# Kernel optimization log

Hardware: AMD Instinct MI355X
Metric: run time of the kernel (lower is better)

## Reference

```python
import jax, jax.numpy as jnp
import numpy as np

EMB_DIM = 2048
N_Q_HEADS = 32
N_KV_HEADS = 8
HEAD_DIM = EMB_DIM // N_Q_HEADS  # 64
N_REP = N_Q_HEADS // N_KV_HEADS  # 4
ROPE_BASE = 10000.0


def setup_inputs() -> dict:
    key = jax.random.key(0)
    ks = jax.random.split(key, 9)
    B, T = 2, 2048
    kv_dim = HEAD_DIM * N_KV_HEADS
    s = 0.02
    return {
        "x":  jax.random.normal(ks[0], (B, T, EMB_DIM), jnp.float32),
        "Wq": jax.random.normal(ks[1], (EMB_DIM, EMB_DIM), jnp.float32) * s,
        "bq": jax.random.normal(ks[2], (EMB_DIM,), jnp.float32) * s,
        "Wk": jax.random.normal(ks[3], (kv_dim, EMB_DIM), jnp.float32) * s,
        "bk": jax.random.normal(ks[4], (kv_dim,), jnp.float32) * s,
        "Wv": jax.random.normal(ks[5], (kv_dim, EMB_DIM), jnp.float32) * s,
        "bv": jax.random.normal(ks[6], (kv_dim,), jnp.float32) * s,
        "Wo": jax.random.normal(ks[7], (EMB_DIM, EMB_DIM), jnp.float32) * s,
        "bo": jax.random.normal(ks[8], (EMB_DIM,), jnp.float32) * s,
    }


def _rope_tables(T, D, dtype):
    inv_freq = 1.0 / (ROPE_BASE ** (jnp.arange(0, D, 2, dtype=jnp.float32) / D))
    t = jnp.arange(T, dtype=jnp.float32)
    freqs = jnp.einsum("i,j->ij", t, inv_freq)          # [T, D/2]
    emb = jnp.concatenate([freqs, freqs], axis=-1)       # [T, D]
    # broadcast over batch and heads: [1, T, 1, D]
    return jnp.cos(emb)[None, :, None, :].astype(dtype), jnp.sin(emb)[None, :, None, :].astype(dtype)


def _rotate_half(x):
    x1, x2 = jnp.split(x, 2, axis=-1)
    return jnp.concatenate([-x2, x1], axis=-1)


def reference(x, Wq, bq, Wk, bk, Wv, bv, Wo, bo):
    B, T, C = x.shape
    q = (x @ Wq.T + bq).reshape(B, T, N_Q_HEADS, HEAD_DIM)
    k = (x @ Wk.T + bk).reshape(B, T, N_KV_HEADS, HEAD_DIM)
    v = (x @ Wv.T + bv).reshape(B, T, N_KV_HEADS, HEAD_DIM)

    cos, sin = _rope_tables(T, HEAD_DIM, x.dtype)
    q = q * cos + _rotate_half(q) * sin
    k = k * cos + _rotate_half(k) * sin

    q = q.transpose(0, 2, 1, 3)                          # [B, Hq, T, D]
    k = k.transpose(0, 2, 1, 3)                          # [B, Hkv, T, D]
    v = v.transpose(0, 2, 1, 3)
    # GQA: repeat_interleave kv heads to match query heads
    k = jnp.repeat(k, N_REP, axis=1)                     # [B, Hq, T, D]
    v = jnp.repeat(v, N_REP, axis=1)

    scale = 1.0 / jnp.sqrt(jnp.asarray(HEAD_DIM, x.dtype))
    att = jnp.einsum("bhqd,bhkd->bhqk", q, k) * scale    # [B, Hq, T, T]
    causal = jnp.tril(jnp.ones((T, T), dtype=bool))
    att = jnp.where(causal[None, None], att, -jnp.inf)
    att = jax.nn.softmax(att, axis=-1)

    y = jnp.einsum("bhqk,bhkd->bhqd", att, v)            # [B, Hq, T, D]
    y = y.transpose(0, 2, 1, 3).reshape(B, T, C)
    return y @ Wo.T + bo
```

## Files before the change

### kernel.cpp

```cpp
#include <hip/hip_runtime.h>
#include <hip/hip_bf16.h>
#include <math.h>


typedef __attribute__((ext_vector_type(8))) short short8;
typedef __attribute__((ext_vector_type(4))) float f32x4;

#define MFMA16(a,b,c) __builtin_amdgcn_mfma_f32_16x16x32_bf16((a),(b),(c),0,0,0)
#define QSCALE 0.18033688011112043f
#define NFREQ  (-13.28771237954945f / 32.0f)

__device__ __forceinline__ ushort f2bf(float f) {
  union { float f; unsigned u; } x; x.f = f;
  unsigned r = x.u + 0x7fffu + ((x.u >> 16) & 1u);
  return (ushort)(r >> 16);
}
__device__ __forceinline__ uint pkbf(float a, float b) {
  union { float f; unsigned u; } x, y; x.f = a; y.f = b;
  return ((x.u + 0x8000u) >> 16) | ((y.u + 0x8000u) & 0xffff0000u);
}

__device__ __forceinline__ void g2l16(const void* g, void* l) {
  __builtin_amdgcn_global_load_lds(
      (__attribute__((address_space(1))) void*)g,
      (__attribute__((address_space(3))) void*)l, 16, 0, 0);
}

__global__ void cvt_all(const float* __restrict__ x,  const float* __restrict__ wq,
                        const float* __restrict__ wk, const float* __restrict__ wv,
                        const float* __restrict__ wo,
                        ushort* __restrict__ x_bf, ushort* __restrict__ wqkv,
                        ushort* __restrict__ wo_bf) {
  int i = blockIdx.x * 256 + threadIdx.x;
  const float4* src; ushort* dst; int off;
  if (i < 2097152)      { src = (const float4*)x;  dst = x_bf;             off = i; }
  else if (i < 3145728) { src = (const float4*)wq; dst = wqkv;             off = i - 2097152; }
  else if (i < 3407872) { src = (const float4*)wk; dst = wqkv + 4194304;   off = i - 3145728; }
  else if (i < 3670016) { src = (const float4*)wv; dst = wqkv + 5242880;   off = i - 3407872; }
  else                  { src = (const float4*)wo; dst = wo_bf;            off = i - 3670016; }
  float4 v = src[off];
  ushort4 o;
  o.x = f2bf(v.x); o.y = f2bf(v.y); o.z = f2bf(v.z); o.w = f2bf(v.w);
  ((ushort4*)dst)[off] = o;
}

__global__ __launch_bounds__(256, 3)
void gemm_qkv(const ushort* __restrict__ A, const ushort* __restrict__ Bw,
              const float* __restrict__ bq, const float* __restrict__ bk,
              const float* __restrict__ bv,
              ushort* __restrict__ qr, ushort* __restrict__ kr,
              ushort* __restrict__ vt) {
  const int K = 2048;
  __shared__ ushort As[2][128*32];
  __shared__ ushort Bs[2][128*32];
  const int tid = threadIdx.x;
  const int wave = tid >> 6, lane = tid & 63;
  const int wm = wave >> 1, wn = wave & 1;
  const int quad = lane >> 4, l16 = lane & 15;
  const int swg = (l16 >> 1) & 3;
  const int m0 = blockIdx.y * 128, n0 = blockIdx.x * 128;

  f32x4 acc[4][4] = {};

  auto stage = [&](int buf, int k0) {
#pragma unroll
    for (int i = 0; i < 2; ++i) {
      int cbase = (i*4 + wave) * 64;
      int p = cbase + lane;
      int row = p >> 2, pcb = p & 3;
      int cl = pcb ^ ((row >> 1) & 3);
      g2l16(A  + (size_t)(m0 + row) * K + k0 + cl * 8, As[buf] + (size_t)cbase * 8);
      g2l16(Bw + (size_t)(n0 + row) * K + k0 + cl * 8, Bs[buf] + (size_t)cbase * 8);
    }
  };

  stage(0, 0);
  for (int k0 = 0; k0 < K; k0 += 32) {
    __syncthreads();
    int cur = (k0 >> 5) & 1;
    if (k0 + 32 < K) stage(cur ^ 1, k0 + 32);

    short8 af[4], bfr[4];
#pragma unroll
    for (int mi = 0; mi < 4; ++mi)
      af[mi] = *(const short8*)(As[cur] + (wm*64 + mi*16 + l16)*32 + ((quad ^ swg) * 8));
#pragma unroll
    for (int ni = 0; ni < 4; ++ni)
      bfr[ni] = *(const short8*)(Bs[cur] + (wn*64 + ni*16 + l16)*32 + ((quad ^ swg) * 8));
#pragma unroll
    for (int mi = 0; mi < 4; ++mi)
#pragma unroll
      for (int ni = 0; ni < 4; ++ni)
        acc[mi][ni] = MFMA16(af[mi], bfr[ni], acc[mi][ni]);
  }

  const int bb = m0 >> 11;
  const int tb = (m0 & 2047) + wm*64;

  if (blockIdx.x < 20) {
    const bool isq = blockIdx.x < 16;
    const float scale = isq ? QSCALE : 1.0f;
#pragma unroll
    for (int ni = 0; ni < 2; ++ni) {
      int n = n0 + wn*64 + ni*16 + l16;
      int d = ni*16 + l16;
      float bias1, bias2;
      ushort* dst;
      if (isq) {
        bias1 = bq[n]; bias2 = bq[n + 32];
        dst = qr + ((size_t)(bb*32 + (n >> 6)) * 2048) * 64 + d;
      } else {
        bias1 = bk[n - 2048]; bias2 = bk[n - 2016];
        dst = kr + ((size_t)(bb*8 + ((n >> 6) - 32)) * 2048) * 64 + d;
      }
      float invf = exp2f((float)d * NFREQ);
#pragma unroll
      for (int mi = 0; mi < 4; ++mi) {
#pragma unroll
        for (int r = 0; r < 4; ++r) {
          int t = tb + mi*16 + quad*4 + r;
          float x1 = acc[mi][ni][r]   + bias1;
          float x2 = acc[mi][ni+2][r] + bias2;
          float f = (float)t * invf;
          float sn = __sinf(f), cs = __cosf(f);
          dst[(size_t)t*64]      = f2bf((x1*cs - x2*sn) * scale);
          dst[(size_t)t*64 + 32] = f2bf((x2*cs + x1*sn) * scale);
        }
      }
    }
  } else {
#pragma unroll
    for (int ni = 0; ni < 4; ++ni) {
      int n = n0 + wn*64 + ni*16 + l16;
      int d = ni*16 + l16;
      float bias = bv[n - 2560];
      ushort* dst = vt + ((size_t)(bb*8 + ((n - 2560) >> 6)) * 64 + d) * 2048;
#pragma unroll
      for (int mi = 0; mi < 4; ++mi) {
        int t = tb + mi*16 + quad*4;
        uint2 pk;
        pk.x = (uint)f2bf(acc[mi][ni][0]+bias) | ((uint)f2bf(acc[mi][ni][1]+bias) << 16);
        pk.y = (uint)f2bf(acc[mi][ni][2]+bias) | ((uint)f2bf(acc[mi][ni][3]+bias) << 16);
        *(uint2*)(dst + t) = pk;
      }
    }
  }
}

__global__ __launch_bounds__(256, 3)
void gemm128(const ushort* __restrict__ A, const ushort* __restrict__ Bw,
             const float* __restrict__ b0,
             float* __restrict__ Cout, int M, int N, int K) {
  __shared__ ushort As[2][128*32];
  __shared__ ushort Bs[2][128*32];
  const int tid = threadIdx.x;
  const int wave = tid >> 6, lane = tid & 63;
  const int wm = wave >> 1, wn = wave & 1;
  const int quad = lane >> 4, l16 = lane & 15;
  const int swg = (l16 >> 1) & 3;
  const int m0 = blockIdx.y * 128, n0 = blockIdx.x * 128;

  f32x4 acc[4][4] = {};

  auto stage = [&](int buf, int k0) {
#pragma unroll
    for (int i = 0; i < 2; ++i) {
      int cbase = (i*4 + wave) * 64;
      int p = cbase + lane;
      int row = p >> 2, pcb = p & 3;
      int cl = pcb ^ ((row >> 1) & 3);
      g2l16(A  + (size_t)(m0 + row) * K + k0 + cl * 8, As[buf] + (size_t)cbase * 8);
      g2l16(Bw + (size_t)(n0 + row) * K + k0 + cl * 8, Bs[buf] + (size_t)cbase * 8);
    }
  };

  stage(0, 0);
  for (int k0 = 0; k0 < K; k0 += 32) {
    __syncthreads();
    int cur = (k0 >> 5) & 1;
    if (k0 + 32 < K) stage(cur ^ 1, k0 + 32);

    short8 af[4], bfr[4];
#pragma unroll
    for (int mi = 0; mi < 4; ++mi)
      af[mi] = *(const short8*)(As[cur] + (wm*64 + mi*16 + l16)*32 + ((quad ^ swg) * 8));
#pragma unroll
    for (int ni = 0; ni < 4; ++ni)
      bfr[ni] = *(const short8*)(Bs[cur] + (wn*64 + ni*16 + l16)*32 + ((quad ^ swg) * 8));
#pragma unroll
    for (int mi = 0; mi < 4; ++mi)
#pragma unroll
      for (int ni = 0; ni < 4; ++ni)
        acc[mi][ni] = MFMA16(af[mi], bfr[ni], acc[mi][ni]);
  }

#pragma unroll
  for (int ni = 0; ni < 4; ++ni) {
    int n = n0 + wn*64 + ni*16 + l16;
    float bias = b0[n];
#pragma unroll
    for (int mi = 0; mi < 4; ++mi) {
#pragma unroll
      for (int r = 0; r < 4; ++r) {
        int m = m0 + wm*64 + mi*16 + quad*4 + r;
        Cout[(size_t)m * N + n] = acc[mi][ni][r] + bias;
      }
    }
  }
}

__global__ __launch_bounds__(256, 4)
void attn(const ushort* __restrict__ Q, const ushort* __restrict__ Kb,
          const ushort* __restrict__ Vt, ushort* __restrict__ Y) {
  __shared__ ushort Ks[2][64*64];
  __shared__ ushort Vs[2][64*64];
  __shared__ ushort Ps[4*16*64];
  const int tid = threadIdx.x, wave = tid >> 6, lane = tid & 63;
  const int quad = lane >> 4, l16 = lane & 15;
  const int h = blockIdx.y, b = blockIdx.z;
  const int hk = h >> 2;
  const ushort* Qb = Q  + ((size_t)(b*32 + h)  * 2048) * 64;
  const ushort* Kg = Kb + ((size_t)(b*8 + hk) * 2048) * 64;
  const ushort* Vg = Vt + ((size_t)(b*8 + hk) * 64) * 2048;
  ushort* Pw = Ps + wave * 1024;
  const int sw = l16 & 7;

  auto stage = [&](int buf, int kt) {
#pragma unroll
    for (int i = 0; i < 2; ++i) {
      int cbase = (i*4 + wave) * 64;
      int p = cbase + lane;
      int row = p >> 3, pcb = p & 7;
      int cl = pcb ^ (row & 7);
      g2l16(Kg + (size_t)(kt*64 + row)*64 + cl*8, Ks[buf] + (size_t)cbase*8);
      g2l16(Vg + (size_t)row*2048 + kt*64 + cl*8, Vs[buf] + (size_t)cbase*8);
    }
  };

  for (int pass = 0; pass < 2; ++pass) {
    const int qt = pass ? (31 - blockIdx.x) : blockIdx.x;
    const int q0 = qt * 64;
    const int qrow = q0 + wave*16 + l16;
    short8 qf0 = *(const short8*)(Qb + (size_t)qrow*64 + quad*8);
    short8 qf1 = *(const short8*)(Qb + (size_t)qrow*64 + 32 + quad*8);

    f32x4 o[4] = {};
    f32x4 l4 = {0.f, 0.f, 0.f, 0.f};

    __syncthreads();
    stage(0, 0);

    for (int kt = 0; kt <= qt; ++kt) {
      __syncthreads();
      int cur = kt & 1;
      if (kt < qt) stage(cur ^ 1, kt + 1);

      f32x4 s[4];
#pragma unroll
      for (int kb = 0; kb < 4; ++kb) {
        const ushort* krow = Ks[cur] + (kb*16 + l16)*64;
        short8 kf0 = *(const short8*)(krow + ((quad       ^ sw) * 8));
        short8 kf1 = *(const short8*)(krow + (((4 + quad) ^ sw) * 8));
        f32x4 z = {0.f, 0.f, 0.f, 0.f};
        z = MFMA16(kf0, qf0, z);
        s[kb] = MFMA16(kf1, qf1, z);
      }

      if (kt == qt) {
        int ql = wave*16 + l16;
#pragma unroll
        for (int kb = 0; kb < 4; ++kb) {
          int keyl = kb*16 + quad*4;
#pragma unroll
          for (int r = 0; r < 4; ++r)
            if (keyl + r > ql) s[kb][r] = -INFINITY;
        }
      }

#pragma unroll
      for (int kb = 0; kb < 4; ++kb)
#pragma unroll
        for (int r = 0; r < 4; ++r)
          s[kb][r] = __builtin_amdgcn_exp2f(s[kb][r]);

      l4 += (s[0] + s[1]) + (s[2] + s[3]);

#pragma unroll
      for (int kb = 0; kb < 4; ++kb) {
        uint2 pk;
        pk.x = pkbf(s[kb][0], s[kb][1]);
        pk.y = pkbf(s[kb][2], s[kb][3]);
        int G = (kb*2 + (quad >> 1)) ^ sw;
        *(uint2*)((char*)Pw + l16*128 + G*16 + (quad & 1)*8) = pk;
      }

#pragma unroll
      for (int kc = 0; kc < 2; ++kc) {
        short8 pf = *(const short8*)((char*)Pw + l16*128 + (((kc*4 + quad) ^ sw) * 16));
#pragma unroll
        for (int db = 0; db < 4; ++db) {
          const ushort* vrow = Vs[cur] + (db*16 + l16)*64;
          short8 vf = *(const short8*)(vrow + (((kc*4 + quad) ^ sw) * 8));
          o[db] = MFMA16(vf, pf, o[db]);
        }
      }
    }

    float l = (l4[0] + l4[1]) + (l4[2] + l4[3]);
    l += __shfl_xor(l, 16);
    l += __shfl_xor(l, 32);
    float inv = 1.0f / l;

    int q = q0 + wave*16 + l16;
#pragma unroll
    for (int db = 0; db < 4; ++db) {
      size_t base = ((size_t)(b*2048 + q)) * 2048 + h*64 + db*16 + quad*4;
      ((uint*)Y)[base >> 1]       = pkbf(o[db][0]*inv, o[db][1]*inv);
      ((uint*)Y)[(base >> 1) + 1] = pkbf(o[db][2]*inv, o[db][3]*inv);
    }
  }
}

extern "C" void kernel_launch(void* const* d_in, const int* in_sizes, int n_in,
                              void* d_out, int out_size, void* d_ws, size_t ws_size,
                              hipStream_t stream) {
  (void)in_sizes; (void)n_in; (void)out_size; (void)ws_size;
  const float* x  = (const float*)d_in[0];
  const float* Wq = (const float*)d_in[1];
  const float* bq = (const float*)d_in[2];
  const float* Wk = (const float*)d_in[3];
  const float* bk = (const float*)d_in[4];
  const float* Wv = (const float*)d_in[5];
  const float* bv = (const float*)d_in[6];
  const float* Wo = (const float*)d_in[7];
  const float* bo = (const float*)d_in[8];
  float* out = (float*)d_out;

  ushort* ws    = (ushort*)d_ws;
  ushort* x_bf  = ws;
  ushort* wqkv  = x_bf + 8388608;
  ushort* wo_bf = wqkv + 6291456;
  ushort* qr    = wo_bf + 4194304;
  ushort* kr    = qr + 8388608;
  ushort* vt    = kr + 2097152;
  ushort* Y     = x_bf;

  cvt_all<<<18432, 256, 0, stream>>>(x, Wq, Wk, Wv, Wo, x_bf, wqkv, wo_bf);
  gemm_qkv<<<dim3(24, 32), 256, 0, stream>>>(x_bf, wqkv, bq, bk, bv, qr, kr, vt);
  attn<<<dim3(16, 32, 2), 256, 0, stream>>>(qr, kr, vt, Y);
  gemm128<<<dim3(16, 32), 256, 0, stream>>>(Y, wo_bf, bo, out, 4096, 2048, 2048);
}
```

Measured before the change: 295.2 us.

## Enlarge attention query tile to 128 rows and remap GEMM block order

The attention kernel moves to 512-thread blocks, each covering 128 query rows with 8 waves. Every staged K/V tile is now shared by twice as many waves, which halves the K/V traffic per query and halves the block count. It also adds s_setprio around the MFMA sections. Both GEMMs gain a block-index swizzle that groups neighbouring tiles to improve L2 reuse. The risks are lower occupancy from the larger blocks and extra masked work on the diagonal, since causal masking now spans two 64-key tiles.

Result: faster. 286.3 us (-3.0%).

```diff
diff --git a/kernel.cpp b/kernel.cpp
--- a/kernel.cpp
+++ b/kernel.cpp
@@ -58,7 +58,10 @@
   const int wm = wave >> 1, wn = wave & 1;
   const int quad = lane >> 4, l16 = lane & 15;
   const int swg = (l16 >> 1) & 3;
-  const int m0 = blockIdx.y * 128, n0 = blockIdx.x * 128;
+  int id = blockIdx.y * 24 + blockIdx.x;
+  id = (id & 7) * 96 + (id >> 3);
+  const int bx = id % 24, by = id / 24;
+  const int m0 = by * 128, n0 = bx * 128;
 
   f32x4 acc[4][4] = {};
 
@@ -97,8 +100,8 @@
   const int bb = m0 >> 11;
   const int tb = (m0 & 2047) + wm*64;
 
-  if (blockIdx.x < 20) {
-    const bool isq = blockIdx.x < 16;
+  if (bx < 20) {
+    const bool isq = bx < 16;
     const float scale = isq ? QSCALE : 1.0f;
 #pragma unroll
     for (int ni = 0; ni < 2; ++ni) {
@@ -158,7 +161,9 @@
   const int wm = wave >> 1, wn = wave & 1;
   const int quad = lane >> 4, l16 = lane & 15;
   const int swg = (l16 >> 1) & 3;
-  const int m0 = blockIdx.y * 128, n0 = blockIdx.x * 128;
+  int id = blockIdx.y * 16 + blockIdx.x;
+  id = (id & 7) * 64 + (id >> 3);
+  const int m0 = (id / 16) * 128, n0 = (id % 16) * 128;
 
   f32x4 acc[4][4] = {};
 
@@ -209,12 +214,12 @@
   }
 }
 
-__global__ __launch_bounds__(256, 4)
+__global__ __launch_bounds__(512, 4)
 void attn(const ushort* __restrict__ Q, const ushort* __restrict__ Kb,
           const ushort* __restrict__ Vt, ushort* __restrict__ Y) {
   __shared__ ushort Ks[2][64*64];
   __shared__ ushort Vs[2][64*64];
-  __shared__ ushort Ps[4*16*64];
+  __shared__ ushort Ps[8*16*64];
   const int tid = threadIdx.x, wave = tid >> 6, lane = tid & 63;
   const int quad = lane >> 4, l16 = lane & 15;
   const int h = blockIdx.y, b = blockIdx.z;
@@ -226,20 +231,16 @@
   const int sw = l16 & 7;
 
   auto stage = [&](int buf, int kt) {
-#pragma unroll
-    for (int i = 0; i < 2; ++i) {
-      int cbase = (i*4 + wave) * 64;
-      int p = cbase + lane;
-      int row = p >> 3, pcb = p & 7;
-      int cl = pcb ^ (row & 7);
-      g2l16(Kg + (size_t)(kt*64 + row)*64 + cl*8, Ks[buf] + (size_t)cbase*8);
-      g2l16(Vg + (size_t)row*2048 + kt*64 + cl*8, Vs[buf] + (size_t)cbase*8);
-    }
+    int p = tid;
+    int row = p >> 3, pcb = p & 7;
+    int cl = pcb ^ (row & 7);
+    g2l16(Kg + (size_t)(kt*64 + row)*64 + cl*8, Ks[buf] + wave*512);
+    g2l16(Vg + (size_t)row*2048 + kt*64 + cl*8, Vs[buf] + wave*512);
   };
 
   for (int pass = 0; pass < 2; ++pass) {
-    const int qt = pass ? (31 - blockIdx.x) : blockIdx.x;
-    const int q0 = qt * 64;
+    const int qt = pass ? (15 - blockIdx.x) : blockIdx.x;
+    const int q0 = qt * 128;
     const int qrow = q0 + wave*16 + l16;
     short8 qf0 = *(const short8*)(Qb + (size_t)qrow*64 + quad*8);
     short8 qf1 = *(const short8*)(Qb + (size_t)qrow*64 + 32 + quad*8);
@@ -250,12 +251,14 @@
     __syncthreads();
     stage(0, 0);
 
-    for (int kt = 0; kt <= qt; ++kt) {
+    const int ktmax = qt*2 + 1;
+    for (int kt = 0; kt <= ktmax; ++kt) {
       __syncthreads();
       int cur = kt & 1;
-      if (kt < qt) stage(cur ^ 1, kt + 1);
+      if (kt < ktmax) stage(cur ^ 1, kt + 1);
 
       f32x4 s[4];
+      __builtin_amdgcn_s_setprio(1);
 #pragma unroll
       for (int kb = 0; kb < 4; ++kb) {
         const ushort* krow = Ks[cur] + (kb*16 + l16)*64;
@@ -265,15 +268,16 @@
         z = MFMA16(kf0, qf0, z);
         s[kb] = MFMA16(kf1, qf1, z);
       }
-
-      if (kt == qt) {
-        int ql = wave*16 + l16;
+      __builtin_amdgcn_s_setprio(0);
+
+      if (kt >= qt*2) {
+        int ql = q0 + wave*16 + l16;
 #pragma unroll
         for (int kb = 0; kb < 4; ++kb) {
-          int keyl = kb*16 + quad*4;
+          int key = kt*64 + kb*16 + quad*4;
 #pragma unroll
           for (int r = 0; r < 4; ++r)
-            if (keyl + r > ql) s[kb][r] = -INFINITY;
+            if (key + r > ql) s[kb][r] = -INFINITY;
         }
       }
 
@@ -294,6 +298,7 @@
         *(uint2*)((char*)Pw + l16*128 + G*16 + (quad & 1)*8) = pk;
       }
 
+      __builtin_amdgcn_s_setprio(1);
 #pragma unroll
       for (int kc = 0; kc < 2; ++kc) {
         short8 pf = *(const short8*)((char*)Pw + l16*128 + (((kc*4 + quad) ^ sw) * 16));
@@ -304,6 +309,7 @@
           o[db] = MFMA16(vf, pf, o[db]);
         }
       }
+      __builtin_amdgcn_s_setprio(0);
     }
 
     float l = (l4[0] + l4[1]) + (l4[2] + l4[3]);
@@ -347,6 +353,6 @@
 
   cvt_all<<<18432, 256, 0, stream>>>(x, Wq, Wk, Wv, Wo, x_bf, wqkv, wo_bf);
   gemm_qkv<<<dim3(24, 32), 256, 0, stream>>>(x_bf, wqkv, bq, bk, bv, qr, kr, vt);
-  attn<<<dim3(16, 32, 2), 256, 0, stream>>>(qr, kr, vt, Y);
+  attn<<<dim3(8, 32, 2), 512, 0, stream>>>(qr, kr, vt, Y);
   gemm128<<<dim3(16, 32), 256, 0, stream>>>(Y, wo_bf, bo, out, 4096, 2048, 2048);
 }
```
